# Optimization experiments

Hardware: AMD Instinct MI355X
Metric: run time of the kernel (lower is better)

## Reference

```python
import jax, jax.numpy as jnp
import numpy as np

B, L, P = 64, 256, 32
LANE_DIM, EMBED, DEPTH, HEADS = 2, 128, 4, 8
MLP = 4 * EMBED
HD = EMBED // HEADS
MASK_RATIO, ELIG = 0.5, 5


def _glorot(key, shape):
    lim = float(np.sqrt(6.0 / (shape[-2] + shape[-1])))
    return jax.random.uniform(key, shape, jnp.float32, -lim, lim)


def setup_inputs() -> dict:
    key = jax.random.key(0)
    ks = jax.random.split(key, 24)
    lane_positions = jax.random.normal(ks[0], (B, L, P, LANE_DIM), jnp.float32)
    lane_centers = jax.random.normal(ks[1], (B, L, LANE_DIM), jnp.float32)
    lane_angles = jax.random.normal(ks[2], (B, L), jnp.float32)
    # ragged padding + random masking, precomputed (externalizes torch randperm loop)
    rng = np.random.default_rng(0)
    pad = rng.random((B, L, P)) < 0.2  # True = padding
    valid = ~pad
    num_valid = valid.sum(-1)                      # (B,L)
    eligible = num_valid > ELIG
    num_mask = (num_valid * MASK_RATIO).astype(np.int32)  # trunc == .int()
    scores = np.where(valid, rng.random((B, L, P)), 2.0)
    rank = scores.argsort(-1).argsort(-1)          # rank of each valid point
    sel = (rank < num_mask[..., None]) & valid & eligible[..., None]
    inp = {
        'lane_positions': lane_positions,
        'lane_centers': lane_centers,
        'lane_angles': lane_angles,
        'lane_padding_mask': jnp.asarray(pad),
        'sel_mask': jnp.asarray(sel),
        'Wp': _glorot(ks[3], (LANE_DIM, EMBED)), 'bp': jnp.zeros((EMBED,)),
        'Wpe1': _glorot(ks[4], (4, EMBED)), 'bpe1': jnp.zeros((EMBED,)),
        'Wpe2': _glorot(ks[5], (EMBED, EMBED)), 'bpe2': jnp.zeros((EMBED,)),
        'lane_type': 0.02 * jax.random.normal(ks[6], (EMBED,), jnp.float32),
        'mask_token': 0.02 * jax.random.normal(ks[7], (EMBED,), jnp.float32),
        'Wqkv': _glorot(ks[8], (DEPTH, EMBED, 3 * EMBED)), 'bqkv': jnp.zeros((DEPTH, 3 * EMBED)),
        'Wo': _glorot(ks[9], (DEPTH, EMBED, EMBED)), 'bo': jnp.zeros((DEPTH, EMBED)),
        'ln1_s': jnp.ones((DEPTH, EMBED)), 'ln1_b': jnp.zeros((DEPTH, EMBED)),
        'Wm1': _glorot(ks[10], (DEPTH, EMBED, MLP)), 'bm1': jnp.zeros((DEPTH, MLP)),
        'Wm2': _glorot(ks[11], (DEPTH, MLP, EMBED)), 'bm2': jnp.zeros((DEPTH, EMBED)),
        'ln2_s': jnp.ones((DEPTH, EMBED)), 'ln2_b': jnp.zeros((DEPTH, EMBED)),
        'lnf_s': jnp.ones((EMBED,)), 'lnf_b': jnp.zeros((EMBED,)),
        'Wd1': _glorot(ks[12], (EMBED, MLP)), 'bd1': jnp.zeros((MLP,)),
        'Wd2': _glorot(ks[13], (MLP, LANE_DIM)), 'bd2': jnp.zeros((LANE_DIM,)),
    }
    return inp


def _ln(x, s, b):
    m = jnp.mean(x, -1, keepdims=True)
    v = jnp.var(x, -1, keepdims=True)
    return (x - m) * jax.lax.rsqrt(v + 1e-5) * s + b


def _forward(lane_positions, lane_centers, lane_angles, Wp, bp, Wpe1, bpe1,
             Wpe2, bpe2, lane_type, mask_token, Wqkv, bqkv, Wo, bo, ln1_s,
             ln1_b, Wm1, bm1, Wm2, bm2, ln2_s, ln2_b, lnf_s, lnf_b, Wd1, bd1,
             Wd2, bd2, sel_mask):
    lane_norm = lane_positions - lane_centers[:, :, None, :]      # (B,L,P,2)
    feat = lane_norm @ Wp + bp                                    # (B,L,P,E)
    pos_feat = jnp.concatenate([lane_centers,
                                jnp.cos(lane_angles)[..., None],
                                jnp.sin(lane_angles)[..., None]], -1)  # (B,L,4)
    pe = jax.nn.gelu(pos_feat @ Wpe1 + bpe1, approximate=False) @ Wpe2 + bpe2
    tok = feat + pe[:, :, None, :] + lane_type
    tok = jnp.where(sel_mask[..., None], mask_token, tok)
    x = tok.reshape(B * L, P, EMBED)
    scale = 1.0 / np.sqrt(HD).astype(np.float32)
    for i in range(DEPTH):  # SpaNet: pre-LN transformer encoder over points
        h = _ln(x, ln1_s[i], ln1_b[i])
        q, k, v = jnp.split(h @ Wqkv[i] + bqkv[i], 3, axis=-1)
        q = q.reshape(B * L, P, HEADS, HD)
        k = k.reshape(B * L, P, HEADS, HD)
        v = v.reshape(B * L, P, HEADS, HD)
        att = jax.nn.softmax(jnp.einsum('nqhd,nkhd->nhqk', q, k) * scale, -1)
        o = jnp.einsum('nhqk,nkhd->nqhd', att, v).reshape(B * L, P, EMBED)
        x = x + o @ Wo[i] + bo[i]
        h = _ln(x, ln2_s[i], ln2_b[i])
        x = x + jax.nn.gelu(h @ Wm1[i] + bm1[i], approximate=False) @ Wm2[i] + bm2[i]
    x = _ln(x, lnf_s, lnf_b)
    y = (jax.nn.relu(x @ Wd1 + bd1) @ Wd2 + bd2).reshape(B, L, P, LANE_DIM)
    selc = sel_mask[..., None].astype(y.dtype)
    sq = (y - lane_norm) ** 2
    loss = jnp.sum(sq * selc) / jnp.maximum(jnp.sum(selc) * LANE_DIM, 1.0)
    return loss, y


def reference(lane_positions, lane_centers, lane_angles, lane_padding_mask,
              sel_mask, Wp, bp, Wpe1, bpe1, Wpe2, bpe2, lane_type, mask_token,
              Wqkv, bqkv, Wo, bo, ln1_s, ln1_b, Wm1, bm1, Wm2, bm2, ln2_s,
              ln2_b, lnf_s, lnf_b, Wd1, bd1, Wd2, bd2):
    del lane_padding_mask  # already folded into sel_mask during setup
    return _forward(lane_positions, lane_centers, lane_angles, Wp, bp, Wpe1,
                    bpe1, Wpe2, bpe2, lane_type, mask_token, Wqkv, bqkv, Wo,
                    bo, ln1_s, ln1_b, Wm1, bm1, Wm2, bm2, ln2_s, ln2_b, lnf_s,
                    lnf_b, Wd1, bd1, Wd2, bd2, sel_mask)
```

## Files before the change

kernel.cpp:

```cpp
#include <hip/hip_runtime.h>


#define NP 32
#define NE 128
#define NSEQ (64 * 256)
#define NMLP 512
#define NDEPTH 4
#define LST 132
#define HBS 136
#define H1C 264
#define VST 40

#define QKV_W_OFF 0
#define O_W_OFF   196608
#define M1_W_OFF  262144
#define M2_W_OFF  524288
#define D1_W_OFF  786432
#define W_TOTAL   851968
#define WS_NEED   (64 + (size_t)W_TOTAL * 2)

typedef unsigned short u16;
typedef unsigned int u32;
typedef __attribute__((ext_vector_type(8))) short bf16x8;
typedef __attribute__((ext_vector_type(4))) float f32x4;
#define MFMA16 __builtin_amdgcn_mfma_f32_16x16x32_bf16

__device__ __forceinline__ float b2f(u16 u) {
  union { u32 i; float f; } v; v.i = ((u32)u) << 16; return v.f;
}
__device__ __forceinline__ u16 f2b(float f) {
  union { float f; u32 i; } v; v.f = f;
  u32 x = v.i;
  x += 0x7fffu + ((x >> 16) & 1u);
  return (u16)(x >> 16);
}
__device__ __forceinline__ u32 pk2(float lo, float hi) {
  return (u32)f2b(lo) | ((u32)f2b(hi) << 16);
}

__device__ __forceinline__ float gelu_f(float x) {
  float z = fabsf(x) * 0.7071067811865476f;
  float t = __builtin_amdgcn_rcpf(fmaf(z, 0.3275911f, 1.0f));
  float poly = t * fmaf(t, fmaf(t, fmaf(t, fmaf(t, 1.061405429f, -1.453152027f),
                        1.421413741f), -0.284496736f), 0.254829592f);
  float e = __expf(-z * z);
  float erf_abs = fmaf(-poly, e, 1.0f);
  float erf = copysignf(erf_abs, x);
  return 0.5f * x * (1.0f + erf);
}

struct Args {
  const float *pos, *ctr, *ang;
  const int *sel;
  const float *Wp, *bp, *Wpe1, *bpe1, *Wpe2, *bpe2, *ltype, *mtok;
  const float *Wqkv, *bqkv, *Wo, *bo, *ln1s, *ln1b, *Wm1, *bm1, *Wm2, *bm2;
  const float *ln2s, *ln2b, *lnfs, *lnfb, *Wd1, *bd1, *Wd2, *bd2;
  float* out;
  float* wsf;
  int* wsi;
};

__global__ void pack_w(const float* __restrict__ src, u16* __restrict__ dst,
                       int K, int N, int L, int scaleN, float scale) {
  int id = blockIdx.x * 256 + threadIdx.x;
  int KT = K >> 5, NT = N >> 4;
  int total = L * NT * KT * 64;
  if (id >= total) return;
  int lane = id & 63;
  int rest = id >> 6;
  int kt = rest % KT;
  int rest2 = rest / KT;
  int nt = rest2 % NT;
  int l = rest2 / NT;
  int col = nt * 16 + (lane & 15);
  float sc = (col < scaleN) ? scale : 1.0f;
  const float* s = src + (size_t)l * K * N + (size_t)(kt * 32 + (lane >> 4) * 8) * N + col;
  u16 tmp[8];
#pragma unroll
  for (int j = 0; j < 8; ++j) tmp[j] = f2b(s[(size_t)j * N] * sc);
  ((uint4*)dst)[id] = *(const uint4*)tmp;
}

template <int NTW>
__device__ __forceinline__ void gemm_kt4_b(const u16* __restrict__ hA, int SA,
                                           const u16* __restrict__ B, int w,
                                           int lane, const float* __restrict__ bias,
                                           f32x4 (&acc)[NTW][2]) {
  int ar = lane & 15, ac = (lane >> 4) * 8;
  bf16x8 af[8];
#pragma unroll
  for (int kb = 0; kb < 4; ++kb) {
    af[kb]     = *(const bf16x8*)(hA + ar * SA + kb * 32 + ac);
    af[kb + 4] = *(const bf16x8*)(hA + (ar + 16) * SA + kb * 32 + ac);
  }
#pragma unroll
  for (int i = 0; i < NTW; ++i) {
    int nt = w + 4 * i;
    const u16* Bp = B + (size_t)nt * 2048 + lane * 8;
    float bb = bias[nt * 16 + ar];
    f32x4 bi = {bb, bb, bb, bb};
    acc[i][0] = bi; acc[i][1] = bi;
#pragma unroll
    for (int kb = 0; kb < 4; ++kb) {
      bf16x8 b = *(const bf16x8*)(Bp + kb * 512);
      acc[i][0] = MFMA16(af[kb], b, acc[i][0], 0, 0, 0);
      acc[i][1] = MFMA16(af[kb + 4], b, acc[i][1], 0, 0, 0);
    }
  }
}

__device__ __forceinline__ void gemm_kt8_acc(const u16* __restrict__ hA,
                                             const u16* __restrict__ B, int ktoff,
                                             int w, int lane, f32x4 (&acc)[2][2]) {
  int ar = lane & 15, ac = (lane >> 4) * 8;
#pragma unroll
  for (int ktl = 0; ktl < 8; ++ktl) {
    bf16x8 a0 = *(const bf16x8*)(hA + ar * H1C + ktl * 32 + ac);
    bf16x8 a1 = *(const bf16x8*)(hA + (ar + 16) * H1C + ktl * 32 + ac);
#pragma unroll
    for (int i = 0; i < 2; ++i) {
      int nt = w + 4 * i;
      bf16x8 b = *(const bf16x8*)(B + (size_t)nt * 8192 + (size_t)(ktoff + ktl) * 512 + lane * 8);
      acc[i][0] = MFMA16(a0, b, acc[i][0], 0, 0, 0);
      acc[i][1] = MFMA16(a1, b, acc[i][1], 0, 0, 0);
    }
  }
}

__device__ __forceinline__ void layer_norm_bf(const float* __restrict__ src,
                                              u16* __restrict__ dst,
                                              const float* gam, const float* bet,
                                              int t, float* mrow, float* vrow) {
  int p = t >> 3, j0 = (t & 7) * 16;
  const float* row = src + p * LST + j0;
  float sum = 0.f, sq = 0.f;
#pragma unroll
  for (int k = 0; k < 16; ++k) { float v = row[k]; sum += v; sq += v * v; }
#pragma unroll
  for (int o = 1; o < 8; o <<= 1) { sum += __shfl_xor(sum, o); sq += __shfl_xor(sq, o); }
  if ((t & 7) == 0) {
    float m = sum * 0.0078125f;
    mrow[p] = m;
    vrow[p] = sq * 0.0078125f - m * m;
  }
  __syncthreads();
  float m = mrow[p], rs = rsqrtf(vrow[p] + 1e-5f);
  u32 wb[8];
#pragma unroll
  for (int k8 = 0; k8 < 4; ++k8) {
    float4 v = ((const float4*)row)[k8];
    float4 g = ((const float4*)(gam + j0))[k8];
    float4 b = ((const float4*)(bet + j0))[k8];
    wb[k8 * 2]     = pk2(fmaf((v.x - m) * rs, g.x, b.x), fmaf((v.y - m) * rs, g.y, b.y));
    wb[k8 * 2 + 1] = pk2(fmaf((v.z - m) * rs, g.z, b.z), fmaf((v.w - m) * rs, g.w, b.w));
  }
  uint4* dp = (uint4*)(dst + p * HBS + j0);
  dp[0] = make_uint4(wb[0], wb[1], wb[2], wb[3]);
  dp[1] = make_uint4(wb[4], wb[5], wb[6], wb[7]);
  __syncthreads();
}

__global__ __launch_bounds__(256, 3) void mrm_main_mfma(Args a, const u16* __restrict__ wsW) {
  __shared__ float xs[32 * LST];
  __shared__ u16 hbf[32 * HBS];
  __shared__ __align__(16) u32 uni4[6656];
  __shared__ float mrow[32], vrow[32];
  __shared__ int selv[32];
  __shared__ float lacc;

  u16* qbuf = (u16*)uni4;
  u16* kbuf = qbuf + 4096;
  u16* vbuf = kbuf + 4096;
  u32* vbuf_w = (u32*)vbuf;
  u16* h1c  = (u16*)uni4;
  float* wd2s = (float*)uni4 + 4224;
  float* tvec = (float*)uni4;
  float* pvec = (float*)uni4 + 128;

  const int s = blockIdx.x;
  const int t = threadIdx.x;
  const int w = t >> 6, lane = t & 63;
  const int cr = lane & 15, rq = (lane >> 4) * 4;
  const int rg = t >> 5, cg = t & 31, r0 = rg * 4, c0 = cg * 4;

  if (t == 0) lacc = 0.f;
  if (t < 32) selv[t] = a.sel[s * NP + t];

  const float cx = a.ctr[s * 2 + 0];
  const float cy = a.ctr[s * 2 + 1];
  const float an = a.ang[s];
  const float ca = cosf(an), sa = sinf(an);

  if (t < 128) {
    float accp = a.bpe1[t] + cx * a.Wpe1[t] + cy * a.Wpe1[128 + t]
               + ca * a.Wpe1[256 + t] + sa * a.Wpe1[384 + t];
    tvec[t] = gelu_f(accp);
  }
  __syncthreads();
  if (t < 128) {
    float accp = a.bpe2[t];
    for (int e = 0; e < 128; ++e) accp += tvec[e] * a.Wpe2[e * 128 + t];
    pvec[t] = accp;
  }
  __syncthreads();

  {
    float4 w0v = *(const float4*)(a.Wp + c0);
    float4 w1v = *(const float4*)(a.Wp + NE + c0);
    float4 bpv = *(const float4*)(a.bp + c0);
    float4 ltv = *(const float4*)(a.ltype + c0);
    float4 mtv = *(const float4*)(a.mtok + c0);
    float a0 = bpv.x + pvec[c0 + 0] + ltv.x;
    float a1 = bpv.y + pvec[c0 + 1] + ltv.y;
    float a2 = bpv.z + pvec[c0 + 2] + ltv.z;
    float a3 = bpv.w + pvec[c0 + 3] + ltv.w;
#pragma unroll
    for (int rr = 0; rr < 4; ++rr) {
      int p = r0 + rr;
      float px = a.pos[(s * NP + p) * 2 + 0] - cx;
      float py = a.pos[(s * NP + p) * 2 + 1] - cy;
      bool mk = selv[p] != 0;
      float4 o;
      o.x = mk ? mtv.x : (px * w0v.x + py * w1v.x + a0);
      o.y = mk ? mtv.y : (px * w0v.y + py * w1v.y + a1);
      o.z = mk ? mtv.z : (px * w0v.z + py * w1v.z + a2);
      o.w = mk ? mtv.w : (px * w0v.w + py * w1v.w + a3);
      *(float4*)&xs[p * LST + c0] = o;
    }
  }
  __syncthreads();

  for (int li = 0; li < NDEPTH; ++li) {
    const u16* qkvW = wsW + QKV_W_OFF + li * 49152;
    const u16* oW   = wsW + O_W_OFF   + li * 16384;
    const u16* m1W  = wsW + M1_W_OFF  + li * 65536;
    const u16* m2W  = wsW + M2_W_OFF  + li * 65536;
    const float* bqkv_i = a.bqkv + li * 384;
    const float* bo_i   = a.bo + li * NE;
    const float* bm1_i  = a.bm1 + li * NMLP;
    const float* bm2_i  = a.bm2 + li * NE;

    layer_norm_bf(xs, hbf, a.ln1s + li * NE, a.ln1b + li * NE, t, mrow, vrow);

    {
      f32x4 acc[6][2];
      {
        int ar = lane & 15, ac = (lane >> 4) * 8;
        bf16x8 af[8];
#pragma unroll
        for (int kb = 0; kb < 4; ++kb) {
          af[kb]     = *(const bf16x8*)(hbf + ar * HBS + kb * 32 + ac);
          af[kb + 4] = *(const bf16x8*)(hbf + (ar + 16) * HBS + kb * 32 + ac);
        }
#pragma unroll
        for (int i = 0; i < 6; ++i) {
          int nt = w + 4 * i;
          const u16* Bp = qkvW + (size_t)nt * 2048 + lane * 8;
          float bb = bqkv_i[nt * 16 + ar];
          if (i < 2) bb *= 0.25f;
          f32x4 bi = {bb, bb, bb, bb};
          acc[i][0] = bi; acc[i][1] = bi;
#pragma unroll
          for (int kb = 0; kb < 4; ++kb) {
            bf16x8 b = *(const bf16x8*)(Bp + kb * 512);
            acc[i][0] = MFMA16(af[kb], b, acc[i][0], 0, 0, 0);
            acc[i][1] = MFMA16(af[kb + 4], b, acc[i][1], 0, 0, 0);
          }
        }
      }
#pragma unroll
      for (int i = 0; i < 6; ++i) {
        int nt = w + 4 * i;
        if (i < 2) {
          u16* qb = qbuf + nt * 512 + cr;
#pragma unroll
          for (int j = 0; j < 4; ++j) {
            qb[(rq + j) * 16]      = f2b(acc[i][0][j]);
            qb[(rq + j + 16) * 16] = f2b(acc[i][1][j]);
          }
        } else if (i < 4) {
          u16* kb = kbuf + (nt - 8) * 512 + cr;
#pragma unroll
          for (int j = 0; j < 4; ++j) {
            kb[(rq + j) * 16]      = f2b(acc[i][0][j]);
            kb[(rq + j + 16) * 16] = f2b(acc[i][1][j]);
          }
        } else {
          u32* vb = vbuf_w + (nt - 16) * 320 + cr * 20 + (rq >> 1);
          vb[0] = pk2(acc[i][0][0], acc[i][0][1]);
          vb[1] = pk2(acc[i][0][2], acc[i][0][3]);
          vb[8] = pk2(acc[i][1][0], acc[i][1][1]);
          vb[9] = pk2(acc[i][1][2], acc[i][1][3]);
        }
      }
    }
    __syncthreads();

    {
      const int l15 = lane & 15, gl = lane >> 4;
      const int bpa_base = (l15 + ((gl & 1) << 5)) << 2;
      const f32x4 z = {0.f, 0.f, 0.f, 0.f};
#pragma unroll
      for (int hi = 0; hi < 2; ++hi) {
        const int h = 2 * w + hi;
        const u16* qb = qbuf + h * 512;
        const u16* kb = kbuf + h * 512;
        bf16x8 vf = *(const bf16x8*)(vbuf + h * 640 + l15 * VST + gl * 8);
        bf16x8 kf0 = {}, kf1 = {};
        if (gl < 2) {
          kf0 = *(const bf16x8*)(kb + l15 * 16 + gl * 8);
          kf1 = *(const bf16x8*)(kb + (16 + l15) * 16 + gl * 8);
        }
#pragma unroll
        for (int qt = 0; qt < 2; ++qt) {
          bf16x8 qf = {};
          if (gl < 2) qf = *(const bf16x8*)(qb + (qt * 16 + l15) * 16 + gl * 8);
          f32x4 s0 = MFMA16(kf0, qf, z, 0, 0, 0);
          f32x4 s1 = MFMA16(kf1, qf, z, 0, 0, 0);
          float mx = fmaxf(fmaxf(fmaxf(s0[0], s0[1]), fmaxf(s0[2], s0[3])),
                           fmaxf(fmaxf(s1[0], s1[1]), fmaxf(s1[2], s1[3])));
          mx = fmaxf(mx, __shfl_xor(mx, 16));
          mx = fmaxf(mx, __shfl_xor(mx, 32));
          float p0 = __expf(s0[0] - mx), p1 = __expf(s0[1] - mx);
          float p2 = __expf(s0[2] - mx), p3 = __expf(s0[3] - mx);
          float p4 = __expf(s1[0] - mx), p5 = __expf(s1[1] - mx);
          float p6 = __expf(s1[2] - mx), p7 = __expf(s1[3] - mx);
          float sum = ((p0 + p1) + (p2 + p3)) + ((p4 + p5) + (p6 + p7));
          sum += __shfl_xor(sum, 16);
          sum += __shfl_xor(sum, 32);
          float inv = 1.f / sum;
          u32 pw0 = pk2(p0 * inv, p1 * inv), pw1 = pk2(p2 * inv, p3 * inv);
          u32 pw2 = pk2(p4 * inv, p5 * inv), pw3 = pk2(p6 * inv, p7 * inv);
          union { u32 uw[4]; bf16x8 v; } pa;
#pragma unroll
          for (int ww = 0; ww < 4; ++ww) {
            int addr = bpa_base + ((ww >> 1) << 6);
            u32 lo = __builtin_amdgcn_ds_bpermute(addr, (int)((ww & 1) ? pw1 : pw0));
            u32 hi2 = __builtin_amdgcn_ds_bpermute(addr, (int)((ww & 1) ? pw3 : pw2));
            pa.uw[ww] = (gl < 2) ? lo : hi2;
          }
          f32x4 o = MFMA16(pa.v, vf, z, 0, 0, 0);
#pragma unroll
          for (int j = 0; j < 4; ++j)
            hbf[(qt * 16 + gl * 4 + j) * HBS + h * 16 + l15] = f2b(o[j]);
        }
      }
    }
    __syncthreads();

    {
      f32x4 acc[2][2];
      gemm_kt4_b<2>(hbf, HBS, oW, w, lane, bo_i, acc);
#pragma unroll
      for (int i = 0; i < 2; ++i) {
        int n = (w + 4 * i) * 16 + cr;
#pragma unroll
        for (int j = 0; j < 4; ++j) {
          xs[(rq + j) * LST + n]      += acc[i][0][j];
          xs[(rq + j + 16) * LST + n] += acc[i][1][j];
        }
      }
    }
    __syncthreads();

    layer_norm_bf(xs, hbf, a.ln2s + li * NE, a.ln2b + li * NE, t, mrow, vrow);

    {
      f32x4 acc2[2][2];
#pragma unroll
      for (int i = 0; i < 2; ++i) {
        float bb = bm2_i[(w + 4 * i) * 16 + cr];
        f32x4 bi = {bb, bb, bb, bb};
        acc2[i][0] = bi; acc2[i][1] = bi;
      }
#pragma unroll
      for (int ch = 0; ch < 2; ++ch) {
        {
          f32x4 acc[4][2];
          gemm_kt4_b<4>(hbf, HBS, m1W + ch * 32768, w, lane, bm1_i + ch * 256, acc);
#pragma unroll
          for (int i = 0; i < 4; ++i) {
            int nl = (w + 4 * i) * 16 + cr;
#pragma unroll
            for (int j = 0; j < 4; ++j) {
              h1c[(rq + j) * H1C + nl]      = f2b(gelu_f(acc[i][0][j]));
              h1c[(rq + j + 16) * H1C + nl] = f2b(gelu_f(acc[i][1][j]));
            }
          }
        }
        __syncthreads();
        gemm_kt8_acc(h1c, m2W, ch * 8, w, lane, acc2);
        __syncthreads();
      }
#pragma unroll
      for (int i = 0; i < 2; ++i) {
        int n = (w + 4 * i) * 16 + cr;
#pragma unroll
        for (int j = 0; j < 4; ++j) {
          xs[(rq + j) * LST + n]      += acc2[i][0][j];
          xs[(rq + j + 16) * LST + n] += acc2[i][1][j];
        }
      }
    }
    __syncthreads();
  }

  layer_norm_bf(xs, hbf, a.lnfs, a.lnfb, t, mrow, vrow);

  for (int i = t; i < 1024; i += 256) wd2s[i] = a.Wd2[i];

  float yacc = 0.f;
  const int pdec = t >> 3, dd2 = (t >> 2) & 1, q4 = t & 3;
#pragma unroll
  for (int ch = 0; ch < 2; ++ch) {
    {
      f32x4 acc[4][2];
      gemm_kt4_b<4>(hbf, HBS, wsW + D1_W_OFF + ch * 32768, w, lane, a.bd1 + ch * 256, acc);
#pragma unroll
      for (int i = 0; i < 4; ++i) {
        int nl = (w + 4 * i) * 16 + cr;
#pragma unroll
        for (int j = 0; j < 4; ++j) {
          h1c[(rq + j) * H1C + nl]      = f2b(fmaxf(acc[i][0][j], 0.f));
          h1c[(rq + j + 16) * H1C + nl] = f2b(fmaxf(acc[i][1][j], 0.f));
        }
      }
    }
    __syncthreads();
    {
      const u16* hrow = h1c + pdec * H1C + q4 * 64;
      const float* wp = wd2s + (ch * 256 + q4 * 64) * 2 + dd2;
#pragma unroll
      for (int k8 = 0; k8 < 8; ++k8) {
        bf16x8 hv = *(const bf16x8*)(hrow + k8 * 8);
#pragma unroll
        for (int jj = 0; jj < 8; ++jj)
          yacc += b2f((u16)hv[jj]) * wp[(k8 * 8 + jj) * 2];
      }
    }
    __syncthreads();
  }

  {
    yacc += __shfl_xor(yacc, 1);
    yacc += __shfl_xor(yacc, 2);
    if (q4 == 0) {
      float y = yacc + a.bd2[dd2];
      a.out[1 + (s * NP + pdec) * 2 + dd2] = y;
      float lnm = a.pos[(s * NP + pdec) * 2 + dd2] - (dd2 ? cy : cx);
      float d = y - lnm;
      if (selv[pdec] != 0) atomicAdd(&lacc, d * d);
    }
  }
  __syncthreads();
  if (t == 0) {
    atomicAdd(a.wsf, lacc);
    int cnt = 0;
#pragma unroll
    for (int p = 0; p < NP; ++p) cnt += (selv[p] != 0) ? 1 : 0;
    atomicAdd(a.wsi, cnt);
  }
}

__global__ void mrm_fin(const float* ws, float* out) {
  float num = ws[0];
  int cnt = ((const int*)ws)[1];
  float den = fmaxf((float)cnt * 2.0f, 1.0f);
  out[0] = num / den;
}

extern "C" void kernel_launch(void* const* d_in, const int* in_sizes, int n_in,
                              void* d_out, int out_size, void* d_ws, size_t ws_size,
                              hipStream_t stream) {
  (void)in_sizes; (void)n_in; (void)out_size; (void)ws_size;
  Args a;
  a.pos   = (const float*)d_in[0];
  a.ctr   = (const float*)d_in[1];
  a.ang   = (const float*)d_in[2];
  a.sel   = (const int*)d_in[4];
  a.Wp    = (const float*)d_in[5];
  a.bp    = (const float*)d_in[6];
  a.Wpe1  = (const float*)d_in[7];
  a.bpe1  = (const float*)d_in[8];
  a.Wpe2  = (const float*)d_in[9];
  a.bpe2  = (const float*)d_in[10];
  a.ltype = (const float*)d_in[11];
  a.mtok  = (const float*)d_in[12];
  a.Wqkv  = (const float*)d_in[13];
  a.bqkv  = (const float*)d_in[14];
  a.Wo    = (const float*)d_in[15];
  a.bo    = (const float*)d_in[16];
  a.ln1s  = (const float*)d_in[17];
  a.ln1b  = (const float*)d_in[18];
  a.Wm1   = (const float*)d_in[19];
  a.bm1   = (const float*)d_in[20];
  a.Wm2   = (const float*)d_in[21];
  a.bm2   = (const float*)d_in[22];
  a.ln2s  = (const float*)d_in[23];
  a.ln2b  = (const float*)d_in[24];
  a.lnfs  = (const float*)d_in[25];
  a.lnfb  = (const float*)d_in[26];
  a.Wd1   = (const float*)d_in[27];
  a.bd1   = (const float*)d_in[28];
  a.Wd2   = (const float*)d_in[29];
  a.bd2   = (const float*)d_in[30];
  a.out   = (float*)d_out;
  a.wsf   = (float*)d_ws;
  a.wsi   = ((int*)d_ws) + 1;

  hipMemsetAsync(d_ws, 0, 8, stream);
  u16* wsW = (u16*)((char*)d_ws + 64);
  pack_w<<<dim3(96),  dim3(256), 0, stream>>>(a.Wqkv, wsW + QKV_W_OFF, 128, 384, 4, 128, 0.25f);
  pack_w<<<dim3(32),  dim3(256), 0, stream>>>(a.Wo,   wsW + O_W_OFF,   128, 128, 4, 0, 1.f);
  pack_w<<<dim3(128), dim3(256), 0, stream>>>(a.Wm1,  wsW + M1_W_OFF,  128, 512, 4, 0, 1.f);
  pack_w<<<dim3(128), dim3(256), 0, stream>>>(a.Wm2,  wsW + M2_W_OFF,  512, 128, 4, 0, 1.f);
  pack_w<<<dim3(32),  dim3(256), 0, stream>>>(a.Wd1,  wsW + D1_W_OFF,  128, 512, 1, 0, 1.f);
  mrm_main_mfma<<<dim3(NSEQ), dim3(256), 0, stream>>>(a, wsW);
  mrm_fin<<<dim3(1), dim3(1), 0, stream>>>((const float*)d_ws, (float*)d_out);
}
```

Baseline: 2.377 ms.

## Shrink LDS footprint, restructure attention per head with 32x32 MFMA

Restructures the attention so that each wave computes Q/K/V for one head at a time into small per-wave buffers. Scores come from a single 32x32x16 MFMA, and probabilities are staged through LDS instead of ds_bpermute. The MLP and decoder hidden chunks are halved (four chunks of 128 rather than two of 256) so the intermediate buffer shares the HBS stride, which cuts shared memory use. Launch bounds are raised from 3 to 4 blocks per CU to exploit this. In exchange there are more barriers and MLP chunk iterations, and possibly register pressure under the tighter occupancy target.

```diff
diff --git a/kernel.cpp b/kernel.cpp
--- a/kernel.cpp
+++ b/kernel.cpp
@@ -8,7 +8,6 @@
 #define NDEPTH 4
 #define LST 132
 #define HBS 136
-#define H1C 264
 #define VST 40
 
 #define QKV_W_OFF 0
@@ -17,13 +16,14 @@
 #define M2_W_OFF  524288
 #define D1_W_OFF  786432
 #define W_TOTAL   851968
-#define WS_NEED   (64 + (size_t)W_TOTAL * 2)
 
 typedef unsigned short u16;
 typedef unsigned int u32;
 typedef __attribute__((ext_vector_type(8))) short bf16x8;
 typedef __attribute__((ext_vector_type(4))) float f32x4;
+typedef __attribute__((ext_vector_type(16))) float f32x16;
 #define MFMA16 __builtin_amdgcn_mfma_f32_16x16x32_bf16
+#define MFMA32 __builtin_amdgcn_mfma_f32_32x32x16_bf16
 
 __device__ __forceinline__ float b2f(u16 u) {
   union { u32 i; float f; } v; v.i = ((u32)u) << 16; return v.f;
@@ -44,8 +44,7 @@
   float poly = t * fmaf(t, fmaf(t, fmaf(t, fmaf(t, 1.061405429f, -1.453152027f),
                         1.421413741f), -0.284496736f), 0.254829592f);
   float e = __expf(-z * z);
-  float erf_abs = fmaf(-poly, e, 1.0f);
-  float erf = copysignf(erf_abs, x);
+  float erf = copysignf(fmaf(-poly, e, 1.0f), x);
   return 0.5f * x * (1.0f + erf);
 }
 
@@ -82,7 +81,7 @@
 }
 
 template <int NTW>
-__device__ __forceinline__ void gemm_kt4_b(const u16* __restrict__ hA, int SA,
+__device__ __forceinline__ void gemm_kt4_b(const u16* __restrict__ hA,
                                            const u16* __restrict__ B, int w,
                                            int lane, const float* __restrict__ bias,
                                            f32x4 (&acc)[NTW][2]) {
@@ -90,8 +89,8 @@
   bf16x8 af[8];
 #pragma unroll
   for (int kb = 0; kb < 4; ++kb) {
-    af[kb]     = *(const bf16x8*)(hA + ar * SA + kb * 32 + ac);
-    af[kb + 4] = *(const bf16x8*)(hA + (ar + 16) * SA + kb * 32 + ac);
+    af[kb]     = *(const bf16x8*)(hA + ar * HBS + kb * 32 + ac);
+    af[kb + 4] = *(const bf16x8*)(hA + (ar + 16) * HBS + kb * 32 + ac);
   }
 #pragma unroll
   for (int i = 0; i < NTW; ++i) {
@@ -109,14 +108,14 @@
   }
 }
 
-__device__ __forceinline__ void gemm_kt8_acc(const u16* __restrict__ hA,
+__device__ __forceinline__ void gemm_kt4_acc(const u16* __restrict__ hA,
                                              const u16* __restrict__ B, int ktoff,
                                              int w, int lane, f32x4 (&acc)[2][2]) {
   int ar = lane & 15, ac = (lane >> 4) * 8;
 #pragma unroll
-  for (int ktl = 0; ktl < 8; ++ktl) {
-    bf16x8 a0 = *(const bf16x8*)(hA + ar * H1C + ktl * 32 + ac);
-    bf16x8 a1 = *(const bf16x8*)(hA + (ar + 16) * H1C + ktl * 32 + ac);
+  for (int ktl = 0; ktl < 4; ++ktl) {
+    bf16x8 a0 = *(const bf16x8*)(hA + ar * HBS + ktl * 32 + ac);
+    bf16x8 a1 = *(const bf16x8*)(hA + (ar + 16) * HBS + ktl * 32 + ac);
 #pragma unroll
     for (int i = 0; i < 2; ++i) {
       int nt = w + 4 * i;
@@ -160,28 +159,26 @@
   __syncthreads();
 }
 
-__global__ __launch_bounds__(256, 3) void mrm_main_mfma(Args a, const u16* __restrict__ wsW) {
+__global__ __launch_bounds__(256, 4) void mrm_main_mfma(Args a, const u16* __restrict__ wsW) {
   __shared__ float xs[32 * LST];
-  __shared__ u16 hbf[32 * HBS];
-  __shared__ __align__(16) u32 uni4[6656];
+  __shared__ __align__(16) u16 hbf[32 * HBS];
+  __shared__ __align__(16) u16 uniu[6656];
   __shared__ float mrow[32], vrow[32];
   __shared__ int selv[32];
   __shared__ float lacc;
 
-  u16* qbuf = (u16*)uni4;
-  u16* kbuf = qbuf + 4096;
-  u16* vbuf = kbuf + 4096;
-  u32* vbuf_w = (u32*)vbuf;
-  u16* h1c  = (u16*)uni4;
-  float* wd2s = (float*)uni4 + 4224;
-  float* tvec = (float*)uni4;
-  float* pvec = (float*)uni4 + 128;
+  u16* h1c = uniu;
+  float* wd2s = (float*)(uniu + 4608);
+  float* tvec = (float*)uniu;
+  float* pvec = (float*)uniu + 128;
 
   const int s = blockIdx.x;
   const int t = threadIdx.x;
   const int w = t >> 6, lane = t & 63;
   const int cr = lane & 15, rq = (lane >> 4) * 4;
   const int rg = t >> 5, cg = t & 31, r0 = rg * 4, c0 = cg * 4;
+  const int l15 = lane & 15, gl = lane >> 4;
+  const int l31 = lane & 31, hi5 = lane >> 5;
 
   if (t == 0) lacc = 0.f;
   if (t < 32) selv[t] = a.sel[s * NP + t];
@@ -230,6 +227,10 @@
   }
   __syncthreads();
 
+  u16* qb2 = uniu + w * 512;
+  u16* kb2 = uniu + 2048 + w * 512;
+  u16* vb2 = uniu + 4096 + w * 640;
+
   for (int li = 0; li < NDEPTH; ++li) {
     const u16* qkvW = wsW + QKV_W_OFF + li * 49152;
     const u16* oW   = wsW + O_W_OFF   + li * 16384;
@@ -242,22 +243,29 @@
 
     layer_norm_bf(xs, hbf, a.ln1s + li * NE, a.ln1b + li * NE, t, mrow, vrow);
 
+    bf16x8 af[8];
     {
-      f32x4 acc[6][2];
+      int ar = lane & 15, ac = (lane >> 4) * 8;
+#pragma unroll
+      for (int kb = 0; kb < 4; ++kb) {
+        af[kb]     = *(const bf16x8*)(hbf + ar * HBS + kb * 32 + ac);
+        af[kb + 4] = *(const bf16x8*)(hbf + (ar + 16) * HBS + kb * 32 + ac);
+      }
+    }
+    __syncthreads();
+
+#pragma unroll
+    for (int p = 0; p < 2; ++p) {
+      const int hh = 4 * p + w;
+      f32x4 acc[3][2];
       {
-        int ar = lane & 15, ac = (lane >> 4) * 8;
-        bf16x8 af[8];
-#pragma unroll
-        for (int kb = 0; kb < 4; ++kb) {
-          af[kb]     = *(const bf16x8*)(hbf + ar * HBS + kb * 32 + ac);
-          af[kb + 4] = *(const bf16x8*)(hbf + (ar + 16) * HBS + kb * 32 + ac);
-        }
-#pragma unroll
-        for (int i = 0; i < 6; ++i) {
-          int nt = w + 4 * i;
+        int ar = lane & 15;
+#pragma unroll
+        for (int i = 0; i < 3; ++i) {
+          int nt = i * 8 + hh;
           const u16* Bp = qkvW + (size_t)nt * 2048 + lane * 8;
           float bb = bqkv_i[nt * 16 + ar];
-          if (i < 2) bb *= 0.25f;
+          if (i == 0) bb *= 0.25f;
           f32x4 bi = {bb, bb, bb, bb};
           acc[i][0] = bi; acc[i][1] = bi;
 #pragma unroll
@@ -268,81 +276,50 @@
           }
         }
       }
-#pragma unroll
-      for (int i = 0; i < 6; ++i) {
-        int nt = w + 4 * i;
-        if (i < 2) {
-          u16* qb = qbuf + nt * 512 + cr;
-#pragma unroll
-          for (int j = 0; j < 4; ++j) {
-            qb[(rq + j) * 16]      = f2b(acc[i][0][j]);
-            qb[(rq + j + 16) * 16] = f2b(acc[i][1][j]);
-          }
-        } else if (i < 4) {
-          u16* kb = kbuf + (nt - 8) * 512 + cr;
-#pragma unroll
-          for (int j = 0; j < 4; ++j) {
-            kb[(rq + j) * 16]      = f2b(acc[i][0][j]);
-            kb[(rq + j + 16) * 16] = f2b(acc[i][1][j]);
-          }
-        } else {
-          u32* vb = vbuf_w + (nt - 16) * 320 + cr * 20 + (rq >> 1);
-          vb[0] = pk2(acc[i][0][0], acc[i][0][1]);
-          vb[1] = pk2(acc[i][0][2], acc[i][0][3]);
-          vb[8] = pk2(acc[i][1][0], acc[i][1][1]);
-          vb[9] = pk2(acc[i][1][2], acc[i][1][3]);
-        }
-      }
-    }
-    __syncthreads();
-
-    {
-      const int l15 = lane & 15, gl = lane >> 4;
-      const int bpa_base = (l15 + ((gl & 1) << 5)) << 2;
-      const f32x4 z = {0.f, 0.f, 0.f, 0.f};
-#pragma unroll
-      for (int hi = 0; hi < 2; ++hi) {
-        const int h = 2 * w + hi;
-        const u16* qb = qbuf + h * 512;
-        const u16* kb = kbuf + h * 512;
-        bf16x8 vf = *(const bf16x8*)(vbuf + h * 640 + l15 * VST + gl * 8);
-        bf16x8 kf0 = {}, kf1 = {};
-        if (gl < 2) {
-          kf0 = *(const bf16x8*)(kb + l15 * 16 + gl * 8);
-          kf1 = *(const bf16x8*)(kb + (16 + l15) * 16 + gl * 8);
-        }
+      {
+#pragma unroll
+        for (int j = 0; j < 4; ++j) {
+          qb2[(rq + j) * 16 + cr]      = f2b(acc[0][0][j]);
+          qb2[(rq + j + 16) * 16 + cr] = f2b(acc[0][1][j]);
+          kb2[(rq + j) * 16 + cr]      = f2b(acc[1][0][j]);
+          kb2[(rq + j + 16) * 16 + cr] = f2b(acc[1][1][j]);
+        }
+        u32* vbw = (u32*)vb2 + cr * 20 + (rq >> 1);
+        vbw[0] = pk2(acc[2][0][0], acc[2][0][1]);
+        vbw[1] = pk2(acc[2][0][2], acc[2][0][3]);
+        vbw[8] = pk2(acc[2][1][0], acc[2][1][1]);
+        vbw[9] = pk2(acc[2][1][2], acc[2][1][3]);
+      }
+      {
+        bf16x8 kf = *(const bf16x8*)(kb2 + l31 * 16 + hi5 * 8);
+        bf16x8 qf = *(const bf16x8*)(qb2 + l31 * 16 + hi5 * 8);
+        f32x16 z16 = {0.f,0.f,0.f,0.f,0.f,0.f,0.f,0.f,0.f,0.f,0.f,0.f,0.f,0.f,0.f,0.f};
+        f32x16 S = MFMA32(kf, qf, z16, 0, 0, 0);
+        float pr[16];
+        float mx = S[0];
+#pragma unroll
+        for (int r = 1; r < 16; ++r) mx = fmaxf(mx, S[r]);
+        mx = fmaxf(mx, __shfl_xor(mx, 32));
+        float sum = 0.f;
+#pragma unroll
+        for (int r = 0; r < 16; ++r) { pr[r] = __expf(S[r] - mx); sum += pr[r]; }
+        sum += __shfl_xor(sum, 32);
+        float inv = 1.f / sum;
+        u16* pb = ((l31 < 16) ? qb2 : kb2) + (l31 & 15) * 32;
+#pragma unroll
+        for (int i2 = 0; i2 < 8; ++i2) {
+          int key0 = ((2 * i2) & 3) + 8 * (i2 >> 1) + 4 * hi5;
+          *(u32*)(pb + key0) = pk2(pr[2 * i2] * inv, pr[2 * i2 + 1] * inv);
+        }
+        bf16x8 vf = *(const bf16x8*)(vb2 + l15 * VST + gl * 8);
+        const f32x4 z = {0.f, 0.f, 0.f, 0.f};
 #pragma unroll
         for (int qt = 0; qt < 2; ++qt) {
-          bf16x8 qf = {};
-          if (gl < 2) qf = *(const bf16x8*)(qb + (qt * 16 + l15) * 16 + gl * 8);
-          f32x4 s0 = MFMA16(kf0, qf, z, 0, 0, 0);
-          f32x4 s1 = MFMA16(kf1, qf, z, 0, 0, 0);
-          float mx = fmaxf(fmaxf(fmaxf(s0[0], s0[1]), fmaxf(s0[2], s0[3])),
-                           fmaxf(fmaxf(s1[0], s1[1]), fmaxf(s1[2], s1[3])));
-          mx = fmaxf(mx, __shfl_xor(mx, 16));
-          mx = fmaxf(mx, __shfl_xor(mx, 32));
-          float p0 = __expf(s0[0] - mx), p1 = __expf(s0[1] - mx);
-          float p2 = __expf(s0[2] - mx), p3 = __expf(s0[3] - mx);
-          float p4 = __expf(s1[0] - mx), p5 = __expf(s1[1] - mx);
-          float p6 = __expf(s1[2] - mx), p7 = __expf(s1[3] - mx);
-          float sum = ((p0 + p1) + (p2 + p3)) + ((p4 + p5) + (p6 + p7));
-          sum += __shfl_xor(sum, 16);
-          sum += __shfl_xor(sum, 32);
-          float inv = 1.f / sum;
-          u32 pw0 = pk2(p0 * inv, p1 * inv), pw1 = pk2(p2 * inv, p3 * inv);
-          u32 pw2 = pk2(p4 * inv, p5 * inv), pw3 = pk2(p6 * inv, p7 * inv);
-          union { u32 uw[4]; bf16x8 v; } pa;
-#pragma unroll
-          for (int ww = 0; ww < 4; ++ww) {
-            int addr = bpa_base + ((ww >> 1) << 6);
-            u32 lo = __builtin_amdgcn_ds_bpermute(addr, (int)((ww & 1) ? pw1 : pw0));
-            u32 hi2 = __builtin_amdgcn_ds_bpermute(addr, (int)((ww & 1) ? pw3 : pw2));
-            pa.uw[ww] = (gl < 2) ? lo : hi2;
-          }
-          f32x4 o = MFMA16(pa.v, vf, z, 0, 0, 0);
+          bf16x8 pa = *(const bf16x8*)(((qt == 0) ? qb2 : kb2) + l15 * 32 + gl * 8);
+          f32x4 o = MFMA16(pa, vf, z, 0, 0, 0);
 #pragma unroll
           for (int j = 0; j < 4; ++j)
-            hbf[(qt * 16 + gl * 4 + j) * HBS + h * 16 + l15] = f2b(o[j]);
+            hbf[(qt * 16 + gl * 4 + j) * HBS + hh * 16 + l15] = f2b(o[j]);
         }
       }
     }
@@ -350,7 +327,7 @@
 
     {
       f32x4 acc[2][2];
-      gemm_kt4_b<2>(hbf, HBS, oW, w, lane, bo_i, acc);
+      gemm_kt4_b<2>(hbf, oW, w, lane, bo_i, acc);
 #pragma unroll
       for (int i = 0; i < 2; ++i) {
         int n = (w + 4 * i) * 16 + cr;
@@ -374,22 +351,22 @@
         acc2[i][0] = bi; acc2[i][1] = bi;
       }
 #pragma unroll
-      for (int ch = 0; ch < 2; ++ch) {
+      for (int ch = 0; ch < 4; ++ch) {
         {
-          f32x4 acc[4][2];
-          gemm_kt4_b<4>(hbf, HBS, m1W + ch * 32768, w, lane, bm1_i + ch * 256, acc);
-#pragma unroll
-          for (int i = 0; i < 4; ++i) {
+          f32x4 acc[2][2];
+          gemm_kt4_b<2>(hbf, m1W + ch * 16384, w, lane, bm1_i + ch * 128, acc);
+#pragma unroll
+          for (int i = 0; i < 2; ++i) {
             int nl = (w + 4 * i) * 16 + cr;
 #pragma unroll
             for (int j = 0; j < 4; ++j) {
-              h1c[(rq + j) * H1C + nl]      = f2b(gelu_f(acc[i][0][j]));
-              h1c[(rq + j + 16) * H1C + nl] = f2b(gelu_f(acc[i][1][j]));
+              h1c[(rq + j) * HBS + nl]      = f2b(gelu_f(acc[i][0][j]));
+              h1c[(rq + j + 16) * HBS + nl] = f2b(gelu_f(acc[i][1][j]));
             }
           }
         }
         __syncthreads();
-        gemm_kt8_acc(h1c, m2W, ch * 8, w, lane, acc2);
+        gemm_kt4_acc(h1c, m2W, ch * 4, w, lane, acc2);
         __syncthreads();
       }
 #pragma unroll
@@ -412,26 +389,26 @@
   float yacc = 0.f;
   const int pdec = t >> 3, dd2 = (t >> 2) & 1, q4 = t & 3;
 #pragma unroll
-  for (int ch = 0; ch < 2; ++ch) {
+  for (int ch = 0; ch < 4; ++ch) {
     {
-      f32x4 acc[4][2];
-      gemm_kt4_b<4>(hbf, HBS, wsW + D1_W_OFF + ch * 32768, w, lane, a.bd1 + ch * 256, acc);
-#pragma unroll
-      for (int i = 0; i < 4; ++i) {
+      f32x4 acc[2][2];
+      gemm_kt4_b<2>(hbf, wsW + D1_W_OFF + ch * 16384, w, lane, a.bd1 + ch * 128, acc);
+#pragma unroll
+      for (int i = 0; i < 2; ++i) {
         int nl = (w + 4 * i) * 16 + cr;
 #pragma unroll
         for (int j = 0; j < 4; ++j) {
-          h1c[(rq + j) * H1C + nl]      = f2b(fmaxf(acc[i][0][j], 0.f));
-          h1c[(rq + j + 16) * H1C + nl] = f2b(fmaxf(acc[i][1][j], 0.f));
+          h1c[(rq + j) * HBS + nl]      = f2b(fmaxf(acc[i][0][j], 0.f));
+          h1c[(rq + j + 16) * HBS + nl] = f2b(fmaxf(acc[i][1][j], 0.f));
         }
       }
     }
     __syncthreads();
     {
-      const u16* hrow = h1c + pdec * H1C + q4 * 64;
-      const float* wp = wd2s + (ch * 256 + q4 * 64) * 2 + dd2;
-#pragma unroll
-      for (int k8 = 0; k8 < 8; ++k8) {
+      const u16* hrow = h1c + pdec * HBS + q4 * 32;
+      const float* wp = wd2s + (ch * 128 + q4 * 32) * 2 + dd2;
+#pragma unroll
+      for (int k8 = 0; k8 < 4; ++k8) {
         bf16x8 hv = *(const bf16x8*)(hrow + k8 * 8);
 #pragma unroll
         for (int jj = 0; jj < 8; ++jj)
```

Measured after the change: 2.973 ms. +25.1%, slower.
